# Optimization experiments

Hardware: AMD Instinct MI355X
Metric: run time of the kernel (lower is better)

## Reference

```python
import jax, jax.numpy as jnp
import numpy as np

B, S, D, F = 32, 512, 1024, 4096
R_COMMON, R_DOMAIN, E = 16, 16, 8
ALPHA = 2.0


def setup_inputs() -> dict:
    key = jax.random.key(0)
    ks = jax.random.split(key, 12)
    sd = lambda k, shape: jax.random.normal(k, shape, dtype=jnp.float32) * (1.0 / np.sqrt(shape[-1]))
    return {
        "hidden_states": jax.random.normal(ks[0], (B, S, D), dtype=jnp.float32),
        "expert_ids": jax.random.randint(ks[1], (B,), 0, E, dtype=jnp.int32),
        # nn.Linear weights: [out_features, in_features]
        "wi": sd(ks[2], (F, D)),
        "wo": sd(ks[3], (D, F)),
        "common_wi_a": sd(ks[4], (R_COMMON, D)),
        "common_wi_b": sd(ks[5], (F, R_COMMON)),
        "common_wo_a": sd(ks[6], (R_COMMON, F)),
        "common_wo_b": sd(ks[7], (D, R_COMMON)),
        # stacked per-expert LoRA weights
        "experts_wi_a": sd(ks[8], (E, R_DOMAIN, D)),
        "experts_wi_b": sd(ks[9], (F, R_DOMAIN)) * jnp.ones((E, 1, 1)) * 0.0 + sd(ks[9], (E, F, R_DOMAIN)),
        "experts_wo_a": sd(ks[10], (E, R_DOMAIN, F)),
        "experts_wo_b": sd(ks[11], (E, D, R_DOMAIN)),
    }


def _expert_lora(x, expert_ids, Wa, Wb):
    """Per-row (dim 0) expert LoRA correction, vectorized via gather.

    x: [B, S, din]; Wa: [E, r, din]; Wb: [E, dout, r].
    Equivalent to the per-expert mask-gather/scatter-add loop since each
    row belongs to exactly one expert.
    """
    Ab = Wa[expert_ids]  # [B, r, din]
    Bb = Wb[expert_ids]  # [B, dout, r]
    low = jnp.einsum("bsd,brd->bsr", x, Ab)
    return ALPHA * jnp.einsum("bsr,bor->bso", low, Bb)


def reference(hidden_states, expert_ids, wi, wo,
              common_wi_a, common_wi_b, common_wo_a, common_wo_b,
              experts_wi_a, experts_wi_b, experts_wo_a, experts_wo_b):
    x = hidden_states
    hidden_i = jnp.einsum("bsd,fd->bsf", x, wi)
    hidden_i += ALPHA * jnp.einsum("bsr,fr->bsf", jnp.einsum("bsd,rd->bsr", x, common_wi_a), common_wi_b)
    hidden_i += _expert_lora(x, expert_ids, experts_wi_a, experts_wi_b)
    hidden_i = jax.nn.relu(hidden_i)  # dense_act_fn='relu'; dropout is identity (eval)
    hidden_o = jnp.einsum("bsf,df->bsd", hidden_i, wo)
    hidden_o += ALPHA * jnp.einsum("bsr,dr->bsd", jnp.einsum("bsf,rf->bsr", hidden_i, common_wo_a), common_wo_b)
    hidden_o += _expert_lora(hidden_i, expert_ids, experts_wo_a, experts_wo_b)
    return hidden_o
```

## Files before the change

kernel.cpp:

```cpp
#include <hip/hip_runtime.h>
#include <hip/hip_bf16.h>
#include <stdint.h>

#define B_ 32
#define S_ 512
#define D_ 1024
#define F_ 4096
#define N_ (B_*S_)
#define E_ 8
#define ALPHA_ 2.0f

#define LDA1 1088
#define LDA2 4160

typedef __hip_bfloat16 bf16;
typedef __attribute__((ext_vector_type(8))) short short8;
typedef __attribute__((ext_vector_type(8))) __bf16 bf16x8;
typedef __attribute__((ext_vector_type(4))) float f32x4;

__device__ __forceinline__ f32x4 mfma_bf16(short8 a, short8 b, f32x4 c) {
    return __builtin_amdgcn_mfma_f32_16x16x32_bf16(
        __builtin_bit_cast(bf16x8, a), __builtin_bit_cast(bf16x8, b), c, 0, 0, 0);
}

__device__ __forceinline__ void gload_lds16(const void* g, void* l) {
    __builtin_amdgcn_global_load_lds((const __attribute__((address_space(1))) void*)g,
                                     (__attribute__((address_space(3))) void*)l, 16, 0, 0);
}

__device__ __forceinline__ unsigned pack2(float a, float b) {
    unsigned short x = __builtin_bit_cast(unsigned short, __float2bfloat16(a));
    unsigned short y = __builtin_bit_cast(unsigned short, __float2bfloat16(b));
    return (unsigned)x | ((unsigned)y << 16);
}
__device__ __forceinline__ uint2 pack4(float4 v) {
    return make_uint2(pack2(v.x, v.y), pack2(v.z, v.w));
}

__global__ __launch_bounds__(256) void prep_w_kernel(
    const float* __restrict__ wi, const float* __restrict__ wo,
    const float* __restrict__ cwia, const float* __restrict__ cwib,
    const float* __restrict__ cwoa, const float* __restrict__ cwob,
    const float* __restrict__ ewia, const float* __restrict__ ewib,
    const float* __restrict__ ewoa, const float* __restrict__ ewob,
    bf16* __restrict__ wi_b, bf16* __restrict__ wo_b,
    bf16* __restrict__ ex1, bf16* __restrict__ ex2,
    bf16* __restrict__ wilo, bf16* __restrict__ wolo)
{
    const int tid0 = blockIdx.x * blockDim.x + threadIdx.x;
    const int stride = gridDim.x * blockDim.x;

    for (int i = tid0; i < F_*D_/4; i += stride) {
        ((uint2*)wi_b)[i] = pack4(((const float4*)wi)[i]);
        ((uint2*)wo_b)[i] = pack4(((const float4*)wo)[i]);
    }
    for (int i = tid0; i < E_*F_*16; i += stride) {
        int e = i >> 16; int rem = i & 0xFFFF; int f = rem >> 4; int r = rem & 15;
        bf16* dst = ex1 + (((size_t)e*F_ + f) << 6);
        dst[r]      = __float2bfloat16(cwib[f*16 + r]);
        dst[16 + r] = __float2bfloat16(ewib[(((size_t)e*F_ + f) << 4) + r]);
        dst[32 + r] = __float2bfloat16(0.f);
        dst[48 + r] = __float2bfloat16(0.f);
    }
    for (int i = tid0; i < E_*D_*16; i += stride) {
        int e = i >> 14; int rem = i & 0x3FFF; int d = rem >> 4; int r = rem & 15;
        bf16* dst = ex2 + (((size_t)e*D_ + d) << 6);
        dst[r]      = __float2bfloat16(cwob[d*16 + r]);
        dst[16 + r] = __float2bfloat16(ewob[(((size_t)e*D_ + d) << 4) + r]);
        dst[32 + r] = __float2bfloat16(0.f);
        dst[48 + r] = __float2bfloat16(0.f);
    }
    for (int i = tid0; i < E_*32*(D_/4); i += stride) {
        int e = i / (32*(D_/4)); int rem = i - e*(32*(D_/4));
        int r = rem / (D_/4); int c4 = (rem % (D_/4)) * 4;
        const float* src = (r < 16) ? (cwia + (size_t)r*D_ + c4)
                                    : (ewia + ((size_t)(e*16 + (r-16)))*D_ + c4);
        *(uint2*)(wilo + ((size_t)(e*32 + r))*D_ + c4) = pack4(*(const float4*)src);
    }
    for (int i = tid0; i < E_*32*(F_/4); i += stride) {
        int e = i / (32*(F_/4)); int rem = i - e*(32*(F_/4));
        int r = rem / (F_/4); int c4 = (rem % (F_/4)) * 4;
        const float* src = (r < 16) ? (cwoa + (size_t)r*F_ + c4)
                                    : (ewoa + ((size_t)(e*16 + (r-16)))*F_ + c4);
        *(uint2*)(wolo + ((size_t)(e*32 + r))*F_ + c4) = pack4(*(const float4*)src);
    }
}

__global__ __launch_bounds__(256) void prep_x_kernel(
    const float* __restrict__ x, bf16* __restrict__ A1)
{
    const int tid0 = blockIdx.x * blockDim.x + threadIdx.x;
    const int stride = gridDim.x * blockDim.x;
    for (int i = tid0; i < N_*(D_/4); i += stride) {
        int row = i >> 8; int c4 = (i & 255) << 2;
        float4 v = *(const float4*)(x + (size_t)i * 4);
        *(uint2*)(A1 + (size_t)row*LDA1 + c4) = pack4(v);
    }
    for (int i = tid0; i < N_*8; i += stride) {
        int row = i >> 3; int c = (i & 7) << 2;
        *(uint2*)(A1 + (size_t)row*LDA1 + 1056 + c) = make_uint2(0u, 0u);
    }
}

template<int K>
__global__ __launch_bounds__(256) void lowproj_kernel(
    const bf16* __restrict__ A, const bf16* __restrict__ W,
    const int* __restrict__ eids, bf16* __restrict__ Out,
    int lda, int kout)
{
    constexpr int BM = 64, BK = 64;
    __shared__ __align__(16) bf16 Asm[BM*BK];
    __shared__ __align__(16) bf16 Wsm[32*BK];

    const int tid = threadIdx.x;
    const int row0 = blockIdx.x * BM;
    const int e = eids[row0 >> 9];
    const int w = tid >> 6, lane = tid & 63;
    const int tr = tid >> 3, ts = tid & 7;
    const int lrow = lane & 15;
    const int lk16 = (lane >> 4) << 4;

    f32x4 acc[2] = {};

    int aoff, woff[2];
    { int r = w*16 + lrow; aoff = r*128 + (lk16 ^ ((r & 7) << 4)); }
    #pragma unroll
    for (int n = 0; n < 2; ++n) {
        int r = n*16 + lrow; woff[n] = r*128 + (lk16 ^ ((r & 7) << 4));
    }
    const bf16* Wp = W + (size_t)e * 32 * K;

    #pragma unroll 1
    for (int kt = 0; kt < K/BK; ++kt) {
        const int k0 = kt * BK;
        #pragma unroll
        for (int i = 0; i < 2; ++i) {
            int row = tr + 32*i;
            int slot = ts ^ (row & 7);
            gload_lds16(A + (size_t)(row0 + row)*lda + k0 + slot*8,
                        (char*)Asm + row*128 + ts*16);
        }
        {
            int row = tr;
            int slot = ts ^ (row & 7);
            gload_lds16(Wp + (size_t)row*K + k0 + slot*8,
                        (char*)Wsm + row*128 + ts*16);
        }
        __syncthreads();
        #pragma unroll
        for (int kk = 0; kk < 2; ++kk) {
            short8 a = *(const short8*)((const char*)Asm + (aoff ^ (kk << 6)));
            #pragma unroll
            for (int n = 0; n < 2; ++n) {
                short8 b = *(const short8*)((const char*)Wsm + (woff[n] ^ (kk << 6)));
                acc[n] = mfma_bf16(a, b, acc[n]);
            }
        }
        __syncthreads();
    }

    const int jrow = (lane >> 4) << 2;
    #pragma unroll
    for (int n = 0; n < 2; ++n) {
        #pragma unroll
        for (int j = 0; j < 4; ++j) {
            int r = row0 + w*16 + jrow + j;
            int c = n*16 + lrow;
            Out[(size_t)r*lda + kout + c] = __float2bfloat16(ALPHA_ * acc[n][j]);
        }
    }
    #pragma unroll
    for (int i = 0; i < 8; ++i) {
        int idx = tid*8 + i;
        int r = idx >> 5, c = idx & 31;
        Out[(size_t)(row0 + r)*lda + kout + 32 + c] = __float2bfloat16(0.f);
    }
}

template<int KMAIN_IT, int LDAp, int LDBp, int LDCp, int NCOLS, bool RELU_BF16>
__global__ __launch_bounds__(256) void gemm_kernel(
    const bf16* __restrict__ A, const bf16* __restrict__ Bmain,
    const bf16* __restrict__ Bextra, const int* __restrict__ eids,
    void* __restrict__ C)
{
    constexpr int BM = 128, BN = 128, BK = 64;
    __shared__ __align__(16) bf16 Asm[BM*BK];
    __shared__ __align__(16) bf16 Bsm[BN*BK];

    const int tid = threadIdx.x;
    const int arow0 = blockIdx.x * BM;
    const int bcol0 = blockIdx.y * BN;
    const int e = eids[arow0 >> 9];

    const int w = tid >> 6, lane = tid & 63;
    const int wm = w >> 1, wn = w & 1;
    const int tr = tid >> 3, ts = tid & 7;
    const int lrow = lane & 15;
    const int lk16 = (lane >> 4) << 4;

    f32x4 acc[4][4] = {};

    int aoff[4], boff[4];
    #pragma unroll
    for (int m = 0; m < 4; ++m) {
        int ra = wm*64 + m*16 + lrow;
        aoff[m] = ra*128 + (lk16 ^ ((ra & 7) << 4));
        int rb = wn*64 + m*16 + lrow;
        boff[m] = rb*128 + (lk16 ^ ((rb & 7) << 4));
    }

    #pragma unroll 1
    for (int kt = 0; kt < KMAIN_IT + 1; ++kt) {
        const int k0 = kt * BK;
        #pragma unroll
        for (int i = 0; i < 4; ++i) {
            int row = tr + 32*i;
            int slot = ts ^ (row & 7);
            gload_lds16(A + (size_t)(arow0 + row)*LDAp + k0 + slot*8,
                        (char*)Asm + row*128 + ts*16);
        }
        {
            const bf16* bb; int bld; int bk;
            if (kt < KMAIN_IT) { bb = Bmain; bld = LDBp; bk = k0; }
            else { bb = Bextra + (size_t)e * NCOLS * 64; bld = 64; bk = 0; }
            #pragma unroll
            for (int i = 0; i < 4; ++i) {
                int row = tr + 32*i;
                int slot = ts ^ (row & 7);
                gload_lds16(bb + (size_t)(bcol0 + row)*bld + bk + slot*8,
                            (char*)Bsm + row*128 + ts*16);
            }
        }
        __syncthreads();
        #pragma unroll
        for (int kk = 0; kk < 2; ++kk) {
            short8 af[4], bfr[4];
            #pragma unroll
            for (int m = 0; m < 4; ++m)
                af[m] = *(const short8*)((const char*)Asm + (aoff[m] ^ (kk << 6)));
            #pragma unroll
            for (int n = 0; n < 4; ++n)
                bfr[n] = *(const short8*)((const char*)Bsm + (boff[n] ^ (kk << 6)));
            #pragma unroll
            for (int m = 0; m < 4; ++m)
                #pragma unroll
                for (int n = 0; n < 4; ++n)
                    acc[m][n] = mfma_bf16(af[m], bfr[n], acc[m][n]);
        }
        __syncthreads();
    }

    const int jrow = (lane >> 4) << 2;
    if constexpr (RELU_BF16) {
        bf16* Cb = (bf16*)C;
        #pragma unroll
        for (int m = 0; m < 4; ++m)
            #pragma unroll
            for (int j = 0; j < 4; ++j) {
                size_t rbase = (size_t)(arow0 + wm*64 + m*16 + jrow + j) * LDCp;
                #pragma unroll
                for (int n = 0; n < 4; ++n) {
                    float v = acc[m][n][j];
                    v = v > 0.f ? v : 0.f;
                    Cb[rbase + bcol0 + wn*64 + n*16 + lrow] = __float2bfloat16(v);
                }
            }
    } else {
        float* Cf = (float*)C;
        #pragma unroll
        for (int m = 0; m < 4; ++m)
            #pragma unroll
            for (int j = 0; j < 4; ++j) {
                size_t rbase = (size_t)(arow0 + wm*64 + m*16 + jrow + j) * LDCp;
                #pragma unroll
                for (int n = 0; n < 4; ++n)
                    Cf[rbase + bcol0 + wn*64 + n*16 + lrow] = acc[m][n][j];
            }
    }
}

extern "C" void kernel_launch(void* const* d_in, const int* in_sizes, int n_in,
                              void* d_out, int out_size, void* d_ws, size_t ws_size,
                              hipStream_t stream)
{
    const float* x    = (const float*)d_in[0];
    const int*   eids = (const int*)d_in[1];
    const float* wi   = (const float*)d_in[2];
    const float* wo   = (const float*)d_in[3];
    const float* cwia = (const float*)d_in[4];
    const float* cwib = (const float*)d_in[5];
    const float* cwoa = (const float*)d_in[6];
    const float* cwob = (const float*)d_in[7];
    const float* ewia = (const float*)d_in[8];
    const float* ewib = (const float*)d_in[9];
    const float* ewoa = (const float*)d_in[10];
    const float* ewob = (const float*)d_in[11];

    char* p = (char*)d_ws;
    bf16* A1   = (bf16*)p; p += (size_t)N_*LDA1*sizeof(bf16);
    bf16* A2   = (bf16*)p; p += (size_t)N_*LDA2*sizeof(bf16);
    bf16* wi_b = (bf16*)p; p += (size_t)F_*D_*sizeof(bf16);
    bf16* wo_b = (bf16*)p; p += (size_t)D_*F_*sizeof(bf16);
    bf16* ex1  = (bf16*)p; p += (size_t)E_*F_*64*sizeof(bf16);
    bf16* ex2  = (bf16*)p; p += (size_t)E_*D_*64*sizeof(bf16);
    bf16* wilo = (bf16*)p; p += (size_t)E_*32*D_*sizeof(bf16);
    bf16* wolo = (bf16*)p; p += (size_t)E_*32*F_*sizeof(bf16);

    prep_w_kernel<<<dim3(512), dim3(256), 0, stream>>>(
        wi, wo, cwia, cwib, cwoa, cwob, ewia, ewib, ewoa, ewob,
        wi_b, wo_b, ex1, ex2, wilo, wolo);

    prep_x_kernel<<<dim3(2048), dim3(256), 0, stream>>>(x, A1);

    lowproj_kernel<D_><<<dim3(N_/64), dim3(256), 0, stream>>>(
        A1, wilo, eids, A1, LDA1, D_);

    gemm_kernel<16, LDA1, D_, LDA2, F_, true>
        <<<dim3(N_/128, F_/128), dim3(256), 0, stream>>>(A1, wi_b, ex1, eids, A2);

    lowproj_kernel<F_><<<dim3(N_/64), dim3(256), 0, stream>>>(
        A2, wolo, eids, A2, LDA2, F_);

    gemm_kernel<64, LDA2, F_, D_, D_, false>
        <<<dim3(N_/128, D_/128), dim3(256), 0, stream>>>(A2, wo_b, ex2, eids, d_out);

    (void)in_sizes; (void)n_in; (void)out_size; (void)ws_size;
}
```

Before: 570.2 us.

## Replace 128x128 GEMM with double-buffered 256x256 tile kernel and XCD swizzle

Both big GEMMs move to a new kernel with 256x256 output tiles, 512 threads and an 8x4 MFMA accumulator per wave. LDS is double-buffered so the next K tile's global-to-LDS loads are issued during the current tile's MFMAs, with s_setprio around the MFMA bursts. Blocks are remapped with an XCD-aware swizzle for L2 locality. The larger tiles cut global traffic per FLOP and one barrier per tile is removed, but register pressure and LDS use (128KB) go up sharply and occupancy drops.

```diff
diff --git a/kernel.cpp b/kernel.cpp
--- a/kernel.cpp
+++ b/kernel.cpp
@@ -177,104 +177,152 @@
     }
 }
 
-template<int KMAIN_IT, int LDAp, int LDBp, int LDCp, int NCOLS, bool RELU_BF16>
-__global__ __launch_bounds__(256) void gemm_kernel(
+#define DSREAD(base, off) (*(const short8*)((const char*)(base) + (off)))
+
+#define STAGE4(gptr, ld, ldsbase)                                          \
+    _Pragma("unroll")                                                      \
+    for (int i_ = 0; i_ < 4; ++i_) {                                       \
+        int row_ = tr + 64*i_;                                             \
+        int slot_ = ts ^ (row_ & 7);                                       \
+        gload_lds16((gptr) + (size_t)row_*(ld) + slot_*8,                  \
+                    (char*)(ldsbase) + row_*128 + ts*16);                  \
+    }
+
+#define TILE_BODY(AC, BC, DOSTAGE, AN, BN, KTN)                            \
+  {                                                                        \
+    short8 af[4][2]; short8 bq[4][2];                                      \
+                                     \
+    _Pragma("unroll") for (int m = 0; m < 4; ++m)                          \
+      _Pragma("unroll") for (int kk = 0; kk < 2; ++kk)                     \
+        af[m][kk] = DSREAD(AC, aoff[m] ^ (kk << 6));                       \
+    _Pragma("unroll") for (int n = 0; n < 2; ++n)                          \
+      _Pragma("unroll") for (int kk = 0; kk < 2; ++kk)                     \
+        bq[n][kk] = DSREAD(BC, boff[n] ^ (kk << 6));                       \
+    __builtin_amdgcn_s_setprio(1);                                         \
+    _Pragma("unroll") for (int m = 0; m < 4; ++m)                          \
+      _Pragma("unroll") for (int n = 0; n < 2; ++n)                        \
+        _Pragma("unroll") for (int kk = 0; kk < 2; ++kk)                   \
+          acc[m][n] = mfma_bf16(af[m][kk], bq[n][kk], acc[m][n]);          \
+    __builtin_amdgcn_s_setprio(0);                                         \
+                                                   \
+    _Pragma("unroll") for (int n = 2; n < 4; ++n)                          \
+      _Pragma("unroll") for (int kk = 0; kk < 2; ++kk)                     \
+        bq[n][kk] = DSREAD(BC, boff[n] ^ (kk << 6));                       \
+    __builtin_amdgcn_s_setprio(1);                                         \
+    _Pragma("unroll") for (int m = 0; m < 4; ++m)                          \
+      _Pragma("unroll") for (int n = 2; n < 4; ++n)                        \
+        _Pragma("unroll") for (int kk = 0; kk < 2; ++kk)                   \
+          acc[m][n] = mfma_bf16(af[m][kk], bq[n][kk], acc[m][n]);          \
+    __builtin_amdgcn_s_setprio(0);                                         \
+           \
+    _Pragma("unroll") for (int m = 0; m < 4; ++m)                          \
+      _Pragma("unroll") for (int kk = 0; kk < 2; ++kk)                     \
+        af[m][kk] = DSREAD(AC, aoff[m+4] ^ (kk << 6));                     \
+    if (DOSTAGE) {                                                         \
+        STAGE4(Ag + (size_t)(KTN)*64, LDAe, AN);                           \
+        if ((KTN) < KMAIN_EL/64) { STAGE4(Bg + (size_t)(KTN)*64, LDBe, BN); } \
+        else                     { STAGE4(Bxg, 64, BN); }                  \
+    }                                                                      \
+    __builtin_amdgcn_s_setprio(1);                                         \
+    _Pragma("unroll") for (int m = 0; m < 4; ++m)                          \
+      _Pragma("unroll") for (int n = 0; n < 2; ++n)                        \
+        _Pragma("unroll") for (int kk = 0; kk < 2; ++kk)                   \
+          acc[m+4][n] = mfma_bf16(af[m][kk], bq[n][kk], acc[m+4][n]);      \
+    __builtin_amdgcn_s_setprio(0);                                         \
+                                                             \
+    __builtin_amdgcn_s_setprio(1);                                         \
+    _Pragma("unroll") for (int m = 0; m < 4; ++m)                          \
+      _Pragma("unroll") for (int n = 2; n < 4; ++n)                        \
+        _Pragma("unroll") for (int kk = 0; kk < 2; ++kk)                   \
+          acc[m+4][n] = mfma_bf16(af[m][kk], bq[n][kk], acc[m+4][n]);      \
+    __builtin_amdgcn_s_setprio(0);                                         \
+    __syncthreads();                                                       \
+  }
+
+template<int KMAIN_EL, int LDAe, int LDBe, int LDCe, int NCOLSe, bool RELU_BF16>
+__global__ __launch_bounds__(512, 2) void gemm256_kernel(
     const bf16* __restrict__ A, const bf16* __restrict__ Bmain,
     const bf16* __restrict__ Bextra, const int* __restrict__ eids,
     void* __restrict__ C)
 {
-    constexpr int BM = 128, BN = 128, BK = 64;
-    __shared__ __align__(16) bf16 Asm[BM*BK];
-    __shared__ __align__(16) bf16 Bsm[BN*BK];
+    constexpr int MT = N_/256;
+    constexpr int NT = NCOLSe/256;
+    constexpr int NWG = MT*NT;
+    constexpr int KTILES = KMAIN_EL/64 + 1;
+    static_assert((KTILES & 1) == 1, "pair loop + tail assumes odd KTILES");
+    static_assert(NWG % 8 == 0, "xcd swizzle needs nwg%8==0");
+    constexpr int CPX = NWG/8;
+
+    __shared__ __align__(16) bf16 As[2][256*64];
+    __shared__ __align__(16) bf16 Bs[2][256*64];
+
+    const int bid = blockIdx.x;
+    const int wg = (bid & 7) * CPX + (bid >> 3);
+    const int mt = wg % MT, nt = wg / MT;
+    const int arow0 = mt * 256, bcol0 = nt * 256;
+    const int e = eids[arow0 >> 9];
 
     const int tid = threadIdx.x;
-    const int arow0 = blockIdx.x * BM;
-    const int bcol0 = blockIdx.y * BN;
-    const int e = eids[arow0 >> 9];
-
-    const int w = tid >> 6, lane = tid & 63;
-    const int wm = w >> 1, wn = w & 1;
+    const int lane = tid & 63;
+    const int wid = tid >> 6;
+    const int wm = wid >> 2, wn = wid & 3;
     const int tr = tid >> 3, ts = tid & 7;
-    const int lrow = lane & 15;
+
+    const bf16* Ag  = A + (size_t)arow0 * LDAe;
+    const bf16* Bg  = Bmain + (size_t)bcol0 * LDBe;
+    const bf16* Bxg = Bextra + ((size_t)e * NCOLSe + bcol0) * 64;
+
+    int aoff[8], boff[4];
     const int lk16 = (lane >> 4) << 4;
-
-    f32x4 acc[4][4] = {};
-
-    int aoff[4], boff[4];
-    #pragma unroll
-    for (int m = 0; m < 4; ++m) {
-        int ra = wm*64 + m*16 + lrow;
-        aoff[m] = ra*128 + (lk16 ^ ((ra & 7) << 4));
-        int rb = wn*64 + m*16 + lrow;
-        boff[m] = rb*128 + (lk16 ^ ((rb & 7) << 4));
-    }
+    #pragma unroll
+    for (int m = 0; m < 8; ++m) {
+        int r = wm*128 + m*16 + (lane & 15);
+        aoff[m] = r*128 + (lk16 ^ ((r & 7) << 4));
+    }
+    #pragma unroll
+    for (int n = 0; n < 4; ++n) {
+        int r = wn*64 + n*16 + (lane & 15);
+        boff[n] = r*128 + (lk16 ^ ((r & 7) << 4));
+    }
+
+    f32x4 acc[8][4] = {};
+
+    STAGE4(Ag, LDAe, As[0]);
+    STAGE4(Bg, LDBe, Bs[0]);
+    __syncthreads();
 
     #pragma unroll 1
-    for (int kt = 0; kt < KMAIN_IT + 1; ++kt) {
-        const int k0 = kt * BK;
-        #pragma unroll
-        for (int i = 0; i < 4; ++i) {
-            int row = tr + 32*i;
-            int slot = ts ^ (row & 7);
-            gload_lds16(A + (size_t)(arow0 + row)*LDAp + k0 + slot*8,
-                        (char*)Asm + row*128 + ts*16);
-        }
-        {
-            const bf16* bb; int bld; int bk;
-            if (kt < KMAIN_IT) { bb = Bmain; bld = LDBp; bk = k0; }
-            else { bb = Bextra + (size_t)e * NCOLS * 64; bld = 64; bk = 0; }
-            #pragma unroll
-            for (int i = 0; i < 4; ++i) {
-                int row = tr + 32*i;
-                int slot = ts ^ (row & 7);
-                gload_lds16(bb + (size_t)(bcol0 + row)*bld + bk + slot*8,
-                            (char*)Bsm + row*128 + ts*16);
-            }
-        }
-        __syncthreads();
-        #pragma unroll
-        for (int kk = 0; kk < 2; ++kk) {
-            short8 af[4], bfr[4];
-            #pragma unroll
-            for (int m = 0; m < 4; ++m)
-                af[m] = *(const short8*)((const char*)Asm + (aoff[m] ^ (kk << 6)));
-            #pragma unroll
-            for (int n = 0; n < 4; ++n)
-                bfr[n] = *(const short8*)((const char*)Bsm + (boff[n] ^ (kk << 6)));
-            #pragma unroll
-            for (int m = 0; m < 4; ++m)
-                #pragma unroll
-                for (int n = 0; n < 4; ++n)
-                    acc[m][n] = mfma_bf16(af[m], bfr[n], acc[m][n]);
-        }
-        __syncthreads();
-    }
+    for (int kt = 0; kt < KTILES - 1; kt += 2) {
+        TILE_BODY(As[0], Bs[0], true, As[1], Bs[1], kt + 1);
+        TILE_BODY(As[1], Bs[1], true, As[0], Bs[0], kt + 2);
+    }
+    TILE_BODY(As[0], Bs[0], false, As[1], Bs[1], 0);
 
     const int jrow = (lane >> 4) << 2;
     if constexpr (RELU_BF16) {
         bf16* Cb = (bf16*)C;
         #pragma unroll
-        for (int m = 0; m < 4; ++m)
+        for (int m = 0; m < 8; ++m)
             #pragma unroll
             for (int j = 0; j < 4; ++j) {
-                size_t rbase = (size_t)(arow0 + wm*64 + m*16 + jrow + j) * LDCp;
+                size_t rbase = (size_t)(arow0 + wm*128 + m*16 + jrow + j) * LDCe;
                 #pragma unroll
                 for (int n = 0; n < 4; ++n) {
                     float v = acc[m][n][j];
                     v = v > 0.f ? v : 0.f;
-                    Cb[rbase + bcol0 + wn*64 + n*16 + lrow] = __float2bfloat16(v);
+                    Cb[rbase + bcol0 + wn*64 + n*16 + (lane & 15)] = __float2bfloat16(v);
                 }
             }
     } else {
         float* Cf = (float*)C;
         #pragma unroll
-        for (int m = 0; m < 4; ++m)
+        for (int m = 0; m < 8; ++m)
             #pragma unroll
             for (int j = 0; j < 4; ++j) {
-                size_t rbase = (size_t)(arow0 + wm*64 + m*16 + jrow + j) * LDCp;
+                size_t rbase = (size_t)(arow0 + wm*128 + m*16 + jrow + j) * LDCe;
                 #pragma unroll
                 for (int n = 0; n < 4; ++n)
-                    Cf[rbase + bcol0 + wn*64 + n*16 + lrow] = acc[m][n][j];
+                    Cf[rbase + bcol0 + wn*64 + n*16 + (lane & 15)] = acc[m][n][j];
             }
     }
 }
@@ -315,14 +363,14 @@
     lowproj_kernel<D_><<<dim3(N_/64), dim3(256), 0, stream>>>(
         A1, wilo, eids, A1, LDA1, D_);
 
-    gemm_kernel<16, LDA1, D_, LDA2, F_, true>
-        <<<dim3(N_/128, F_/128), dim3(256), 0, stream>>>(A1, wi_b, ex1, eids, A2);
+    gemm256_kernel<D_, LDA1, D_, LDA2, F_, true>
+        <<<dim3((N_/256)*(F_/256)), dim3(512), 0, stream>>>(A1, wi_b, ex1, eids, A2);
 
     lowproj_kernel<F_><<<dim3(N_/64), dim3(256), 0, stream>>>(
         A2, wolo, eids, A2, LDA2, F_);
 
-    gemm_kernel<64, LDA2, F_, D_, D_, false>
-        <<<dim3(N_/128, D_/128), dim3(256), 0, stream>>>(A2, wo_b, ex2, eids, d_out);
+    gemm256_kernel<F_, LDA2, F_, D_, D_, false>
+        <<<dim3((N_/256)*(D_/256)), dim3(512), 0, stream>>>(A2, wo_b, ex2, eids, d_out);
 
     (void)in_sizes; (void)n_in; (void)out_size; (void)ws_size;
 }
```

Result: faster. 474.5 us (-16.8%).
